# Kernel tuning notes

Measured on AMD Instinct MI355X. Metric: run time of the kernel, lower is better.

Reference implementation:

```python
import jax, jax.numpy as jnp
import numpy as np

NUM_GRAPHS = 256


def _gcn_norm(edge_index, num_nodes):
    # Add self-loops (PyG GCNConv default) and compute symmetric normalization
    loops = jnp.arange(num_nodes, dtype=edge_index.dtype)
    src = jnp.concatenate([edge_index[0], loops])
    dst = jnp.concatenate([edge_index[1], loops])
    deg = jax.ops.segment_sum(jnp.ones_like(dst, dtype=jnp.float32), dst,
                              num_segments=num_nodes)
    dinv = jnp.where(deg > 0, jax.lax.rsqrt(deg), 0.0)
    norm = dinv[src] * dinv[dst]  # [E + N]
    return src, dst, norm


def _gcn_layer(x, W, b, src, dst, norm, num_nodes):
    h = x @ W                      # transform first (cheaper: N x d_out)
    msg = h[src] * norm[:, None]   # gather + per-edge scale  [E+N, d_out]
    agg = jax.ops.segment_sum(msg, dst, num_segments=num_nodes)
    return agg + b


def setup_inputs() -> dict:
    key = jax.random.key(0)
    ks = jax.random.split(key, 12)
    N, E, F_in = 100000, 1600000, 5
    x = jax.random.normal(ks[0], (N, F_in), dtype=jnp.float32)
    edge_index = jax.random.randint(ks[1], (2, E), 0, N, dtype=jnp.int64)
    batch = jnp.sort(jax.random.randint(ks[2], (N,), 0, NUM_GRAPHS, dtype=jnp.int64))

    def glorot(k, fi, fo):
        s = jnp.sqrt(6.0 / (fi + fo))
        return jax.random.uniform(k, (fi, fo), jnp.float32, -s, s)

    return {
        "x": x, "edge_index": edge_index, "batch": batch,
        "W1": glorot(ks[3], F_in, 64), "b1": jnp.zeros((64,), jnp.float32),
        "W2": glorot(ks[4], 64, 128),  "b2": jnp.zeros((128,), jnp.float32),
        "W3": glorot(ks[5], 128, 64),  "b3": jnp.zeros((64,), jnp.float32),
        "Wfc": glorot(ks[6], 64, 1),   "bfc": jnp.zeros((1,), jnp.float32),
    }


def reference(x, edge_index, batch, W1, b1, W2, b2, W3, b3, Wfc, bfc):
    N = x.shape[0]
    src, dst, norm = _gcn_norm(edge_index, N)
    h = jax.nn.relu(_gcn_layer(x, W1, b1, src, dst, norm, N))
    h = jax.nn.relu(_gcn_layer(h, W2, b2, src, dst, norm, N))
    h = jax.nn.relu(_gcn_layer(h, W3, b3, src, dst, norm, N))
    # global mean pool over graph ids
    sums = jax.ops.segment_sum(h, batch, num_segments=NUM_GRAPHS)
    cnts = jax.ops.segment_sum(jnp.ones((N,), jnp.float32), batch,
                               num_segments=NUM_GRAPHS)
    pooled = sums / jnp.maximum(cnts, 1.0)[:, None]   # [G, 64]
    return jax.nn.sigmoid(pooled @ Wfc + bfc)         # [G, 1]
```

## Files before the change

kernel.cpp:

```cpp
#include <hip/hip_runtime.h>
#include <math.h>

#define NG 256
#define NBK 512
#define BCAP 3584

static __device__ __forceinline__ int bucket_lo(int p, int n) {
    return (int)(((long long)p * n + NBK - 1) / NBK);
}

static __device__ __forceinline__ float blo(unsigned u) {
    return __uint_as_float(u << 16);
}
static __device__ __forceinline__ float bhi(unsigned u) {
    return __uint_as_float(u & 0xFFFF0000u);
}
static __device__ __forceinline__ unsigned packbf(float a, float b) {
    unsigned ua = __float_as_uint(a);
    ua = (ua + 0x7FFFu + ((ua >> 16) & 1u)) >> 16;
    unsigned ub = __float_as_uint(b);
    ub = (ub + 0x7FFFu + ((ub >> 16) & 1u)) & 0xFFFF0000u;
    return ua | ub;
}

__global__ void zero_bcur(int* bcur) {
    int i = blockIdx.x * blockDim.x + threadIdx.x;
    if (i < NBK) bcur[i] = i * BCAP;
}

__global__ void bucketA(const int* __restrict__ src, const int* __restrict__ dst,
                        int* bcur, unsigned* stage, int e, int n) {
    __shared__ int cnt[NBK];
    __shared__ int base[NBK];
    int nb = gridDim.x;
    int c0 = (int)((long long)blockIdx.x * e / nb);
    int c1 = (int)((long long)(blockIdx.x + 1) * e / nb);
    for (int k = threadIdx.x; k < NBK; k += blockDim.x) cnt[k] = 0;
    __syncthreads();
    for (int i = c0 + threadIdx.x; i < c1; i += blockDim.x) {
        int d = dst[i];
        int p = (int)((long long)d * NBK / n);
        atomicAdd(&cnt[p], 1);
    }
    __syncthreads();
    for (int k = threadIdx.x; k < NBK; k += blockDim.x)
        base[k] = atomicAdd(&bcur[k], cnt[k]);
    __syncthreads();
    for (int k = threadIdx.x; k < NBK; k += blockDim.x) cnt[k] = 0;
    __syncthreads();
    for (int i = c0 + threadIdx.x; i < c1; i += blockDim.x) {
        int s = src[i], d = dst[i];
        int p = (int)((long long)d * NBK / n);
        int ldst = d - bucket_lo(p, n);
        int lp = atomicAdd(&cnt[p], 1);
        stage[base[p] + lp] = ((unsigned)s << 8) | (unsigned)ldst;
    }
}

__global__ void fillB2(const unsigned* __restrict__ stage,
                       const int* __restrict__ bcur,
                       int* __restrict__ rowptr, float* __restrict__ dinv,
                       int* __restrict__ csrs,
                       const float* __restrict__ x, float* __restrict__ xs,
                       int n, int e) {
    __shared__ int ldeg[256];
    __shared__ int loff[256];
    __shared__ int bstart;
    int p = blockIdx.x;
    int t = threadIdx.x;
    int lo = bucket_lo(p, n), hi = bucket_lo(p + 1, n);
    int nloc = hi - lo;

    {
        int acc = 0;
        for (int k = t; k < p; k += 256) acc += bcur[k] - k * BCAP;
        ldeg[t] = acc;
        __syncthreads();
        for (int off = 128; off > 0; off >>= 1) {
            if (t < off) ldeg[t] += ldeg[t + off];
            __syncthreads();
        }
        if (t == 0) bstart = ldeg[0];
        __syncthreads();
    }

    if (t < 256) ldeg[t] = 0;
    __syncthreads();
    int s0 = p * BCAP, s1 = bcur[p];
    for (int i = s0 + t; i < s1; i += 256)
        atomicAdd(&ldeg[stage[i] & 255u], 1);
    __syncthreads();

    int v = (t < nloc) ? ldeg[t] : 0;
    loff[t] = v;
    __syncthreads();
    for (int off = 1; off < 256; off <<= 1) {
        int u = (t >= off) ? loff[t - off] : 0;
        __syncthreads();
        loff[t] += u;
        __syncthreads();
    }
    if (t < nloc) {
        int start = bstart + loff[t] - v;
        rowptr[lo + t] = start;
        float dv = rsqrtf((float)v + 1.0f);
        dinv[lo + t] = dv;
        const float* xr = x + (size_t)(lo + t) * 5;
        float* xo = xs + (size_t)(lo + t) * 5;
#pragma unroll
        for (int k = 0; k < 5; ++k) xo[k] = xr[k] * dv;
    }
    if (p == NBK - 1 && t == 0) rowptr[n] = e;
    __syncthreads();
    if (t < nloc) ldeg[t] = bstart + loff[t] - v;
    __syncthreads();

    for (int i = s0 + t; i < s1; i += 256) {
        unsigned pk = stage[i];
        int ldst = (int)(pk & 255u);
        int pos = atomicAdd(&ldeg[ldst], 1);
        csrs[pos] = (int)(pk >> 8);
    }
}

__global__ void gather5(const int* __restrict__ rowptr,
                        const int* __restrict__ csrs,
                        const float* __restrict__ dinv,
                        const float* __restrict__ xs,
                        float* __restrict__ z, int n) {
    int i = blockIdx.x * blockDim.x + threadIdx.x;
    if (i >= n) return;
    const float* xr = xs + (size_t)i * 5;
    float4 x4 = *(const float4*)(xr);
    float a0 = x4.x, a1 = x4.y, a2 = x4.z, a3 = x4.w, a4 = xr[4];
    int j = rowptr[i], end = rowptr[i + 1], e1 = end - 1;
    for (; j < end; j += 4) {
        int s[4]; float m[4];
#pragma unroll
        for (int k = 0; k < 4; ++k) {
            int jj = j + k;
            s[k] = csrs[jj <= e1 ? jj : e1];
            m[k] = (jj < end) ? 1.0f : 0.0f;
        }
        float4 r4[4]; float r1[4];
#pragma unroll
        for (int k = 0; k < 4; ++k) {
            const float* r = xs + (size_t)s[k] * 5;
            r4[k] = *(const float4*)(r);
            r1[k] = r[4];
        }
#pragma unroll
        for (int k = 0; k < 4; ++k) {
            a0 = fmaf(m[k], r4[k].x, a0);
            a1 = fmaf(m[k], r4[k].y, a1);
            a2 = fmaf(m[k], r4[k].z, a2);
            a3 = fmaf(m[k], r4[k].w, a3);
            a4 = fmaf(m[k], r1[k], a4);
        }
    }
    float di = dinv[i];
    float* zr = z + (size_t)i * 5;
    zr[0] = a0 * di; zr[1] = a1 * di; zr[2] = a2 * di;
    zr[3] = a3 * di; zr[4] = a4 * di;
}

template<int DOUT, bool BR, bool SCALE, bool OUTBF>
static __device__ __forceinline__ void emit(float o[8], const float* b, int c,
                                            float dsc, void* out, int i) {
    if (BR) {
        float4 b0 = *(const float4*)(b + c * 8);
        float4 b1 = *(const float4*)(b + c * 8 + 4);
        o[0] = fmaxf(o[0] + b0.x, 0.f); o[1] = fmaxf(o[1] + b0.y, 0.f);
        o[2] = fmaxf(o[2] + b0.z, 0.f); o[3] = fmaxf(o[3] + b0.w, 0.f);
        o[4] = fmaxf(o[4] + b1.x, 0.f); o[5] = fmaxf(o[5] + b1.y, 0.f);
        o[6] = fmaxf(o[6] + b1.z, 0.f); o[7] = fmaxf(o[7] + b1.w, 0.f);
    }
    if (SCALE) {
#pragma unroll
        for (int q = 0; q < 8; ++q) o[q] *= dsc;
    }
    if (OUTBF) {
        uint4 pk;
        pk.x = packbf(o[0], o[1]); pk.y = packbf(o[2], o[3]);
        pk.z = packbf(o[4], o[5]); pk.w = packbf(o[6], o[7]);
        *(uint4*)((unsigned*)out + (size_t)i * (DOUT / 2) + c * 4) = pk;
    } else {
        float* op = (float*)out + (size_t)i * DOUT + c * 8;
        float4 o0 = {o[0], o[1], o[2], o[3]};
        float4 o1 = {o[4], o[5], o[6], o[7]};
        *(float4*)(op) = o0;
        *(float4*)(op + 4) = o1;
    }
}

template<int K, int DOUT, bool BR, bool SCALE, bool OUTBF, int NODES>
__global__ void transformB(const float* __restrict__ xin,
                           const float* __restrict__ W,
                           const float* __restrict__ b,
                           const float* __restrict__ dinv,
                           void* __restrict__ out, int n) {
    const int C = DOUT / 8;
    int tid = blockIdx.x * blockDim.x + threadIdx.x;
    int grp = tid / C;
    int c = tid % C;
    int i0 = grp * NODES;
    if (i0 >= n) return;
    float acc[NODES][8];
#pragma unroll
    for (int nn = 0; nn < NODES; ++nn)
#pragma unroll
        for (int q = 0; q < 8; ++q) acc[nn][q] = 0.0f;

    static_assert(K % 4 == 0, "K multiple of 4");
    int idx[NODES];
#pragma unroll
    for (int nn = 0; nn < NODES; ++nn)
        idx[nn] = (i0 + nn < n) ? i0 + nn : n - 1;

    float4 r[NODES];
#pragma unroll
    for (int nn = 0; nn < NODES; ++nn)
        r[nn] = *(const float4*)(xin + (size_t)idx[nn] * K);

    for (int k0 = 0; k0 < K; k0 += 4) {
        float4 rn[NODES];
        if (k0 + 4 < K) {
#pragma unroll
            for (int nn = 0; nn < NODES; ++nn)
                rn[nn] = *(const float4*)(xin + (size_t)idx[nn] * K + k0 + 4);
        }
#pragma unroll
        for (int kk = 0; kk < 4; ++kk) {
            const float* wp = W + (size_t)(k0 + kk) * DOUT + c * 8;
            float4 w0 = *(const float4*)(wp);
            float4 w1 = *(const float4*)(wp + 4);
#pragma unroll
            for (int nn = 0; nn < NODES; ++nn) {
                float v = (&r[nn].x)[kk];
                acc[nn][0] = fmaf(v, w0.x, acc[nn][0]);
                acc[nn][1] = fmaf(v, w0.y, acc[nn][1]);
                acc[nn][2] = fmaf(v, w0.z, acc[nn][2]);
                acc[nn][3] = fmaf(v, w0.w, acc[nn][3]);
                acc[nn][4] = fmaf(v, w1.x, acc[nn][4]);
                acc[nn][5] = fmaf(v, w1.y, acc[nn][5]);
                acc[nn][6] = fmaf(v, w1.z, acc[nn][6]);
                acc[nn][7] = fmaf(v, w1.w, acc[nn][7]);
            }
        }
#pragma unroll
        for (int nn = 0; nn < NODES; ++nn) r[nn] = rn[nn];
    }
#pragma unroll
    for (int nn = 0; nn < NODES; ++nn) {
        if (i0 + nn >= n) break;
        float dsc = SCALE ? dinv[i0 + nn] : 1.0f;
        emit<DOUT, BR, SCALE, OUTBF>(acc[nn], b, c, dsc, out, i0 + nn);
    }
}

template<int DOUT, bool BR, bool SCALE, bool OUTBF, int NODES>
__global__ void transformB5(const float* __restrict__ xin,
                            const float* __restrict__ W,
                            const float* __restrict__ b,
                            const float* __restrict__ dinv,
                            void* __restrict__ out, int n) {
    const int C = DOUT / 8;
    int tid = blockIdx.x * blockDim.x + threadIdx.x;
    int grp = tid / C;
    int c = tid % C;
    int i0 = grp * NODES;
    if (i0 >= n) return;
    float r[NODES][5];
#pragma unroll
    for (int nn = 0; nn < NODES; ++nn) {
        int idx = i0 + nn < n ? i0 + nn : n - 1;
        const float* row = xin + (size_t)idx * 5;
#pragma unroll
        for (int k = 0; k < 5; ++k) r[nn][k] = row[k];
    }
    float acc[NODES][8];
#pragma unroll
    for (int nn = 0; nn < NODES; ++nn)
#pragma unroll
        for (int q = 0; q < 8; ++q) acc[nn][q] = 0.0f;
#pragma unroll
    for (int k = 0; k < 5; ++k) {
        const float* wp = W + (size_t)k * DOUT + c * 8;
        float4 w0 = *(const float4*)(wp);
        float4 w1 = *(const float4*)(wp + 4);
#pragma unroll
        for (int nn = 0; nn < NODES; ++nn) {
            float v = r[nn][k];
            acc[nn][0] = fmaf(v, w0.x, acc[nn][0]);
            acc[nn][1] = fmaf(v, w0.y, acc[nn][1]);
            acc[nn][2] = fmaf(v, w0.z, acc[nn][2]);
            acc[nn][3] = fmaf(v, w0.w, acc[nn][3]);
            acc[nn][4] = fmaf(v, w1.x, acc[nn][4]);
            acc[nn][5] = fmaf(v, w1.y, acc[nn][5]);
            acc[nn][6] = fmaf(v, w1.z, acc[nn][6]);
            acc[nn][7] = fmaf(v, w1.w, acc[nn][7]);
        }
    }
#pragma unroll
    for (int nn = 0; nn < NODES; ++nn) {
        if (i0 + nn >= n) break;
        float dsc = SCALE ? dinv[i0 + nn] : 1.0f;
        emit<DOUT, BR, SCALE, OUTBF>(acc[nn], b, c, dsc, out, i0 + nn);
    }
}

#define ACCA(AA, V) \
    AA[0] += blo(V.x); AA[1] += bhi(V.x); AA[2] += blo(V.y); AA[3] += bhi(V.y); \
    AA[4] += blo(V.z); AA[5] += bhi(V.z); AA[6] += blo(V.w); AA[7] += bhi(V.w);
#define ACCM(AA, V, M) \
    AA[0] = fmaf(M, blo(V.x), AA[0]); AA[1] = fmaf(M, bhi(V.x), AA[1]); \
    AA[2] = fmaf(M, blo(V.y), AA[2]); AA[3] = fmaf(M, bhi(V.y), AA[3]); \
    AA[4] = fmaf(M, blo(V.z), AA[4]); AA[5] = fmaf(M, bhi(V.z), AA[5]); \
    AA[6] = fmaf(M, blo(V.w), AA[6]); AA[7] = fmaf(M, bhi(V.w), AA[7]);

template<bool BR>
__global__ void gatherBF(const int* __restrict__ rowptr,
                         const int* __restrict__ csrs,
                         const float* __restrict__ dinv,
                         const float* __restrict__ b,
                         const unsigned* __restrict__ g,
                         float* __restrict__ z, int n) {
    int tid = blockIdx.x * blockDim.x + threadIdx.x;
    int i = tid >> 3;
    int c = tid & 7;
    if (i >= n) return;
    uint4 sv = *(const uint4*)(g + (size_t)i * 32 + c * 4);
    float a0[8], a1[8], a2[8], a3[8];
    a0[0] = blo(sv.x); a0[1] = bhi(sv.x); a0[2] = blo(sv.y); a0[3] = bhi(sv.y);
    a0[4] = blo(sv.z); a0[5] = bhi(sv.z); a0[6] = blo(sv.w); a0[7] = bhi(sv.w);
#pragma unroll
    for (int q = 0; q < 8; ++q) { a1[q] = 0.0f; a2[q] = 0.0f; a3[q] = 0.0f; }
    int j = rowptr[i], end = rowptr[i + 1];
    for (; j + 8 <= end; j += 8) {
        uint4 v0 = *(const uint4*)(g + (size_t)csrs[j]     * 32 + c * 4);
        uint4 v1 = *(const uint4*)(g + (size_t)csrs[j + 1] * 32 + c * 4);
        uint4 v2 = *(const uint4*)(g + (size_t)csrs[j + 2] * 32 + c * 4);
        uint4 v3 = *(const uint4*)(g + (size_t)csrs[j + 3] * 32 + c * 4);
        uint4 v4 = *(const uint4*)(g + (size_t)csrs[j + 4] * 32 + c * 4);
        uint4 v5 = *(const uint4*)(g + (size_t)csrs[j + 5] * 32 + c * 4);
        uint4 v6 = *(const uint4*)(g + (size_t)csrs[j + 6] * 32 + c * 4);
        uint4 v7 = *(const uint4*)(g + (size_t)csrs[j + 7] * 32 + c * 4);
        ACCA(a0, v0); ACCA(a1, v1); ACCA(a2, v2); ACCA(a3, v3);
        ACCA(a0, v4); ACCA(a1, v5); ACCA(a2, v6); ACCA(a3, v7);
    }
    if (j < end) {
        int e1 = end - 1;
        int sx[8]; float mm[8];
#pragma unroll
        for (int k = 0; k < 8; ++k) {
            int jj = j + k;
            sx[k] = csrs[jj <= e1 ? jj : e1];
            mm[k] = (jj < end) ? 1.0f : 0.0f;
        }
        uint4 v0 = *(const uint4*)(g + (size_t)sx[0] * 32 + c * 4);
        uint4 v1 = *(const uint4*)(g + (size_t)sx[1] * 32 + c * 4);
        uint4 v2 = *(const uint4*)(g + (size_t)sx[2] * 32 + c * 4);
        uint4 v3 = *(const uint4*)(g + (size_t)sx[3] * 32 + c * 4);
        uint4 v4 = *(const uint4*)(g + (size_t)sx[4] * 32 + c * 4);
        uint4 v5 = *(const uint4*)(g + (size_t)sx[5] * 32 + c * 4);
        uint4 v6 = *(const uint4*)(g + (size_t)sx[6] * 32 + c * 4);
        uint4 v7 = *(const uint4*)(g + (size_t)sx[7] * 32 + c * 4);
        ACCM(a0, v0, mm[0]); ACCM(a1, v1, mm[1]);
        ACCM(a2, v2, mm[2]); ACCM(a3, v3, mm[3]);
        ACCM(a0, v4, mm[4]); ACCM(a1, v5, mm[5]);
        ACCM(a2, v6, mm[6]); ACCM(a3, v7, mm[7]);
    }
    float di = dinv[i];
    float o[8];
#pragma unroll
    for (int q = 0; q < 8; ++q) o[q] = di * ((a0[q] + a1[q]) + (a2[q] + a3[q]));
    if (BR) {
        float4 b0 = *(const float4*)(b + c * 8);
        float4 b1 = *(const float4*)(b + c * 8 + 4);
        o[0] = fmaxf(o[0] + b0.x, 0.f); o[1] = fmaxf(o[1] + b0.y, 0.f);
        o[2] = fmaxf(o[2] + b0.z, 0.f); o[3] = fmaxf(o[3] + b0.w, 0.f);
        o[4] = fmaxf(o[4] + b1.x, 0.f); o[5] = fmaxf(o[5] + b1.y, 0.f);
        o[6] = fmaxf(o[6] + b1.z, 0.f); o[7] = fmaxf(o[7] + b1.w, 0.f);
    }
    float* zp = z + (size_t)i * 64 + c * 8;
    float4 z0 = {o[0], o[1], o[2], o[3]};
    float4 z1 = {o[4], o[5], o[6], o[7]};
    *(float4*)(zp) = z0;
    *(float4*)(zp + 4) = z1;
}

__global__ void pool(const float* __restrict__ h3, const int* __restrict__ batch,
                     const float* __restrict__ Wfc, const float* __restrict__ bfc,
                     float* __restrict__ out, int n) {
    int g = blockIdx.x;
    int lane = threadIdx.x & 63;
    int w = threadIdx.x >> 6;
    int lo = 0, hi = n;
    while (lo < hi) { int m = (lo + hi) >> 1; if (batch[m] < g) lo = m + 1; else hi = m; }
    int start = lo;
    hi = n;
    while (lo < hi) { int m = (lo + hi) >> 1; if (batch[m] < g + 1) lo = m + 1; else hi = m; }
    int end = lo;
    float a0 = 0.f, a1 = 0.f, a2 = 0.f, a3 = 0.f;
    int m = start + w;
    for (; m + 12 < end; m += 16) {
        a0 += h3[(size_t)m * 64 + lane];
        a1 += h3[(size_t)(m + 4) * 64 + lane];
        a2 += h3[(size_t)(m + 8) * 64 + lane];
        a3 += h3[(size_t)(m + 12) * 64 + lane];
    }
    for (; m < end; m += 4) a0 += h3[(size_t)m * 64 + lane];
    __shared__ float sh[4][64];
    sh[w][lane] = (a0 + a1) + (a2 + a3);
    __syncthreads();
    if (w == 0) {
        float v = (sh[0][lane] + sh[1][lane]) + (sh[2][lane] + sh[3][lane]);
        float cnt = (float)(end - start);
        v = (v / fmaxf(cnt, 1.0f)) * Wfc[lane];
#pragma unroll
        for (int off = 32; off > 0; off >>= 1) v += __shfl_down(v, off, 64);
        if (lane == 0) out[g] = 1.0f / (1.0f + expf(-(v + bfc[0])));
    }
}

static inline int cdiv(long long a, int b) { return (int)((a + b - 1) / b); }

extern "C" void kernel_launch(void* const* d_in, const int* in_sizes, int n_in,
                              void* d_out, int out_size, void* d_ws, size_t ws_size,
                              hipStream_t stream) {
    const float* x   = (const float*)d_in[0];
    const int*   ei  = (const int*)d_in[1];
    const int*   bat = (const int*)d_in[2];
    const float* W1  = (const float*)d_in[3];
    const float* b1  = (const float*)d_in[4];
    const float* W2  = (const float*)d_in[5];
    const float* b2  = (const float*)d_in[6];
    const float* W3  = (const float*)d_in[7];
    const float* b3  = (const float*)d_in[8];
    const float* Wfc = (const float*)d_in[9];
    const float* bfc = (const float*)d_in[10];
    float* out = (float*)d_out;

    const int N = in_sizes[0] / 5;
    const int E = in_sizes[1] / 2;
    const int* src = ei;
    const int* ds  = ei + E;

    char* wsb = (char*)d_ws;
    size_t off = 0;
#define A256(X) (((X) + (size_t)255) & ~(size_t)255)
    float* dinv   = (float*)(wsb + off); off = A256(off + (size_t)N * 4);
    int*   rowptr = (int*)(wsb + off);   off = A256(off + (size_t)(N + 4) * 4);
    int*   bcur   = (int*)(wsb + off);   off = A256(off + (size_t)NBK * 4);
    int*   csrs   = (int*)(wsb + off);   off = A256(off + (size_t)E * 4);
    float* A      = (float*)(wsb + off); off = A256(off + (size_t)N * 128 * 4);
    float* B      = (float*)(wsb + off);
#undef A256
    unsigned* stage = (unsigned*)A;
    float*    xs    = A + (size_t)(1 << 21);
    float*    z1    = A;
    unsigned* h1bf  = (unsigned*)B;
    float*    z2    = A;
    float*    h2    = B;
    unsigned* t3bf  = (unsigned*)A;
    float*    h3    = B;

    const int Blk = 256;

    zero_bcur<<<2, 256, 0, stream>>>(bcur);
    bucketA<<<256, 256, 0, stream>>>(src, ds, bcur, stage, E, N);
    fillB2<<<NBK, 256, 0, stream>>>(stage, bcur, rowptr, dinv, csrs, x, xs, N, E);

    gather5<<<cdiv(N, Blk), Blk, 0, stream>>>(rowptr, csrs, dinv, xs, z1, N);
    transformB5<64, true, true, true, 2>
        <<<cdiv((long long)cdiv(N, 2) * 8, Blk), Blk, 0, stream>>>(
        z1, W1, b1, dinv, h1bf, N);

    gatherBF<false><<<cdiv((long long)N * 8, Blk), Blk, 0, stream>>>(
        rowptr, csrs, dinv, nullptr, h1bf, z2, N);
    transformB<64, 128, true, false, false, 4>
        <<<cdiv((long long)cdiv(N, 4) * 16, Blk), Blk, 0, stream>>>(
        z2, W2, b2, nullptr, h2, N);

    transformB<128, 64, false, true, true, 4>
        <<<cdiv((long long)cdiv(N, 4) * 8, Blk), Blk, 0, stream>>>(
        h2, W3, nullptr, dinv, t3bf, N);
    gatherBF<true><<<cdiv((long long)N * 8, Blk), Blk, 0, stream>>>(
        rowptr, csrs, dinv, b3, t3bf, h3, N);

    pool<<<NG, 256, 0, stream>>>(h3, bat, Wfc, bfc, out, N);
}
```

Before: 321.2 us.

## Fuse layer-2 gather, W2 transform and W3 transform into one shared-memory kernel

Replaces the separate gatherBF, transformB (64→128) and transformB (128→64) launches with a single layer23 kernel. Each block aggregates 96 nodes into shared memory, applies W2 with bias and ReLU into a bf16 shared buffer, then applies W3 and writes the dinv-scaled bf16 result. This removes the global round trips for z2 (N×64 fp32) and h2 (N×128 fp32) plus two launches. The costs are heavy shared-memory use that limits occupancy, a gather phase that keeps only 256 threads per block busy, and h2 now being rounded to bf16 before the W3 product.

```diff
diff --git a/kernel.cpp b/kernel.cpp
--- a/kernel.cpp
+++ b/kernel.cpp
@@ -4,6 +4,7 @@
 #define NG 256
 #define NBK 512
 #define BCAP 3584
+#define FBN 96
 
 static __device__ __forceinline__ int bucket_lo(int p, int n) {
     return (int)(((long long)p * n + NBK - 1) / NBK);
@@ -193,71 +194,6 @@
     }
 }
 
-template<int K, int DOUT, bool BR, bool SCALE, bool OUTBF, int NODES>
-__global__ void transformB(const float* __restrict__ xin,
-                           const float* __restrict__ W,
-                           const float* __restrict__ b,
-                           const float* __restrict__ dinv,
-                           void* __restrict__ out, int n) {
-    const int C = DOUT / 8;
-    int tid = blockIdx.x * blockDim.x + threadIdx.x;
-    int grp = tid / C;
-    int c = tid % C;
-    int i0 = grp * NODES;
-    if (i0 >= n) return;
-    float acc[NODES][8];
-#pragma unroll
-    for (int nn = 0; nn < NODES; ++nn)
-#pragma unroll
-        for (int q = 0; q < 8; ++q) acc[nn][q] = 0.0f;
-
-    static_assert(K % 4 == 0, "K multiple of 4");
-    int idx[NODES];
-#pragma unroll
-    for (int nn = 0; nn < NODES; ++nn)
-        idx[nn] = (i0 + nn < n) ? i0 + nn : n - 1;
-
-    float4 r[NODES];
-#pragma unroll
-    for (int nn = 0; nn < NODES; ++nn)
-        r[nn] = *(const float4*)(xin + (size_t)idx[nn] * K);
-
-    for (int k0 = 0; k0 < K; k0 += 4) {
-        float4 rn[NODES];
-        if (k0 + 4 < K) {
-#pragma unroll
-            for (int nn = 0; nn < NODES; ++nn)
-                rn[nn] = *(const float4*)(xin + (size_t)idx[nn] * K + k0 + 4);
-        }
-#pragma unroll
-        for (int kk = 0; kk < 4; ++kk) {
-            const float* wp = W + (size_t)(k0 + kk) * DOUT + c * 8;
-            float4 w0 = *(const float4*)(wp);
-            float4 w1 = *(const float4*)(wp + 4);
-#pragma unroll
-            for (int nn = 0; nn < NODES; ++nn) {
-                float v = (&r[nn].x)[kk];
-                acc[nn][0] = fmaf(v, w0.x, acc[nn][0]);
-                acc[nn][1] = fmaf(v, w0.y, acc[nn][1]);
-                acc[nn][2] = fmaf(v, w0.z, acc[nn][2]);
-                acc[nn][3] = fmaf(v, w0.w, acc[nn][3]);
-                acc[nn][4] = fmaf(v, w1.x, acc[nn][4]);
-                acc[nn][5] = fmaf(v, w1.y, acc[nn][5]);
-                acc[nn][6] = fmaf(v, w1.z, acc[nn][6]);
-                acc[nn][7] = fmaf(v, w1.w, acc[nn][7]);
-            }
-        }
-#pragma unroll
-        for (int nn = 0; nn < NODES; ++nn) r[nn] = rn[nn];
-    }
-#pragma unroll
-    for (int nn = 0; nn < NODES; ++nn) {
-        if (i0 + nn >= n) break;
-        float dsc = SCALE ? dinv[i0 + nn] : 1.0f;
-        emit<DOUT, BR, SCALE, OUTBF>(acc[nn], b, c, dsc, out, i0 + nn);
-    }
-}
-
 template<int DOUT, bool BR, bool SCALE, bool OUTBF, int NODES>
 __global__ void transformB5(const float* __restrict__ xin,
                             const float* __restrict__ W,
@@ -318,17 +254,10 @@
     AA[4] = fmaf(M, blo(V.z), AA[4]); AA[5] = fmaf(M, bhi(V.z), AA[5]); \
     AA[6] = fmaf(M, blo(V.w), AA[6]); AA[7] = fmaf(M, bhi(V.w), AA[7]);
 
-template<bool BR>
-__global__ void gatherBF(const int* __restrict__ rowptr,
-                         const int* __restrict__ csrs,
-                         const float* __restrict__ dinv,
-                         const float* __restrict__ b,
-                         const unsigned* __restrict__ g,
-                         float* __restrict__ z, int n) {
-    int tid = blockIdx.x * blockDim.x + threadIdx.x;
-    int i = tid >> 3;
-    int c = tid & 7;
-    if (i >= n) return;
+static __device__ __forceinline__ void gather_row(const int* __restrict__ rowptr,
+                                                  const int* __restrict__ csrs,
+                                                  const unsigned* __restrict__ g,
+                                                  int i, int c, float o[8]) {
     uint4 sv = *(const uint4*)(g + (size_t)i * 32 + c * 4);
     float a0[8], a1[8], a2[8], a3[8];
     a0[0] = blo(sv.x); a0[1] = bhi(sv.x); a0[2] = blo(sv.y); a0[3] = bhi(sv.y);
@@ -370,10 +299,26 @@
         ACCM(a0, v4, mm[4]); ACCM(a1, v5, mm[5]);
         ACCM(a2, v6, mm[6]); ACCM(a3, v7, mm[7]);
     }
+#pragma unroll
+    for (int q = 0; q < 8; ++q) o[q] = (a0[q] + a1[q]) + (a2[q] + a3[q]);
+}
+
+template<bool BR>
+__global__ void gatherBF(const int* __restrict__ rowptr,
+                         const int* __restrict__ csrs,
+                         const float* __restrict__ dinv,
+                         const float* __restrict__ b,
+                         const unsigned* __restrict__ g,
+                         float* __restrict__ z, int n) {
+    int tid = blockIdx.x * blockDim.x + threadIdx.x;
+    int i = tid >> 3;
+    int c = tid & 7;
+    if (i >= n) return;
+    float o[8];
+    gather_row(rowptr, csrs, g, i, c, o);
     float di = dinv[i];
-    float o[8];
-#pragma unroll
-    for (int q = 0; q < 8; ++q) o[q] = di * ((a0[q] + a1[q]) + (a2[q] + a3[q]));
+#pragma unroll
+    for (int q = 0; q < 8; ++q) o[q] *= di;
     if (BR) {
         float4 b0 = *(const float4*)(b + c * 8);
         float4 b1 = *(const float4*)(b + c * 8 + 4);
@@ -387,6 +332,139 @@
     float4 z1 = {o[4], o[5], o[6], o[7]};
     *(float4*)(zp) = z0;
     *(float4*)(zp + 4) = z1;
+}
+
+__global__ void layer23(const int* __restrict__ rowptr,
+                        const int* __restrict__ csrs,
+                        const float* __restrict__ dinv,
+                        const float* __restrict__ b2v,
+                        const unsigned* __restrict__ g,
+                        const float* __restrict__ W2,
+                        const float* __restrict__ W3,
+                        unsigned* __restrict__ t3, int n) {
+    __shared__ float    z2s[FBN][68];
+    __shared__ unsigned h2s[FBN][68];
+    int t = threadIdx.x;
+    int base = blockIdx.x * FBN;
+
+    {
+        int nd = t >> 3, c = t & 7;
+        for (int pass = 0; pass < 3; ++pass) {
+            int lr = pass * 32 + nd;
+            int i = base + lr;
+            if (i < n) {
+                float o[8];
+                gather_row(rowptr, csrs, g, i, c, o);
+                float di = dinv[i];
+                float4 z0 = {o[0] * di, o[1] * di, o[2] * di, o[3] * di};
+                float4 z1 = {o[4] * di, o[5] * di, o[6] * di, o[7] * di};
+                *(float4*)&z2s[lr][c * 8] = z0;
+                *(float4*)&z2s[lr][c * 8 + 4] = z1;
+            }
+        }
+    }
+    __syncthreads();
+
+    {
+        int c2 = t & 15;
+        int ng = t >> 4;
+        float acc[6][8];
+#pragma unroll
+        for (int nn = 0; nn < 6; ++nn)
+#pragma unroll
+            for (int q = 0; q < 8; ++q) acc[nn][q] = 0.0f;
+        for (int k0 = 0; k0 < 64; k0 += 4) {
+            float4 r[6];
+#pragma unroll
+            for (int nn = 0; nn < 6; ++nn)
+                r[nn] = *(const float4*)&z2s[ng + 16 * nn][k0];
+#pragma unroll
+            for (int kk = 0; kk < 4; ++kk) {
+                const float* wp = W2 + (size_t)(k0 + kk) * 128 + c2 * 8;
+                float4 w0 = *(const float4*)(wp);
+                float4 w1 = *(const float4*)(wp + 4);
+#pragma unroll
+                for (int nn = 0; nn < 6; ++nn) {
+                    float v = (&r[nn].x)[kk];
+                    acc[nn][0] = fmaf(v, w0.x, acc[nn][0]);
+                    acc[nn][1] = fmaf(v, w0.y, acc[nn][1]);
+                    acc[nn][2] = fmaf(v, w0.z, acc[nn][2]);
+                    acc[nn][3] = fmaf(v, w0.w, acc[nn][3]);
+                    acc[nn][4] = fmaf(v, w1.x, acc[nn][4]);
+                    acc[nn][5] = fmaf(v, w1.y, acc[nn][5]);
+                    acc[nn][6] = fmaf(v, w1.z, acc[nn][6]);
+                    acc[nn][7] = fmaf(v, w1.w, acc[nn][7]);
+                }
+            }
+        }
+        float4 b0 = *(const float4*)(b2v + c2 * 8);
+        float4 b1 = *(const float4*)(b2v + c2 * 8 + 4);
+#pragma unroll
+        for (int nn = 0; nn < 6; ++nn) {
+            float o[8];
+            o[0] = fmaxf(acc[nn][0] + b0.x, 0.f);
+            o[1] = fmaxf(acc[nn][1] + b0.y, 0.f);
+            o[2] = fmaxf(acc[nn][2] + b0.z, 0.f);
+            o[3] = fmaxf(acc[nn][3] + b0.w, 0.f);
+            o[4] = fmaxf(acc[nn][4] + b1.x, 0.f);
+            o[5] = fmaxf(acc[nn][5] + b1.y, 0.f);
+            o[6] = fmaxf(acc[nn][6] + b1.z, 0.f);
+            o[7] = fmaxf(acc[nn][7] + b1.w, 0.f);
+            uint4 pk;
+            pk.x = packbf(o[0], o[1]); pk.y = packbf(o[2], o[3]);
+            pk.z = packbf(o[4], o[5]); pk.w = packbf(o[6], o[7]);
+            *(uint4*)&h2s[ng + 16 * nn][c2 * 4] = pk;
+        }
+    }
+    __syncthreads();
+
+    {
+        int c3 = t & 7;
+        int ng = t >> 3;
+        float acc[3][8];
+#pragma unroll
+        for (int nn = 0; nn < 3; ++nn)
+#pragma unroll
+            for (int q = 0; q < 8; ++q) acc[nn][q] = 0.0f;
+        for (int k0 = 0; k0 < 128; k0 += 8) {
+            uint4 r[3];
+#pragma unroll
+            for (int nn = 0; nn < 3; ++nn)
+                r[nn] = *(const uint4*)&h2s[ng + 32 * nn][k0 >> 1];
+#pragma unroll
+            for (int kk = 0; kk < 8; ++kk) {
+                const float* wp = W3 + (size_t)(k0 + kk) * 64 + c3 * 8;
+                float4 w0 = *(const float4*)(wp);
+                float4 w1 = *(const float4*)(wp + 4);
+#pragma unroll
+                for (int nn = 0; nn < 3; ++nn) {
+                    unsigned u = (&r[nn].x)[kk >> 1];
+                    float v = (kk & 1) ? bhi(u) : blo(u);
+                    acc[nn][0] = fmaf(v, w0.x, acc[nn][0]);
+                    acc[nn][1] = fmaf(v, w0.y, acc[nn][1]);
+                    acc[nn][2] = fmaf(v, w0.z, acc[nn][2]);
+                    acc[nn][3] = fmaf(v, w0.w, acc[nn][3]);
+                    acc[nn][4] = fmaf(v, w1.x, acc[nn][4]);
+                    acc[nn][5] = fmaf(v, w1.y, acc[nn][5]);
+                    acc[nn][6] = fmaf(v, w1.z, acc[nn][6]);
+                    acc[nn][7] = fmaf(v, w1.w, acc[nn][7]);
+                }
+            }
+        }
+#pragma unroll
+        for (int nn = 0; nn < 3; ++nn) {
+            int i = base + ng + 32 * nn;
+            if (i < n) {
+                float ds = dinv[i];
+                uint4 pk;
+                pk.x = packbf(acc[nn][0] * ds, acc[nn][1] * ds);
+                pk.y = packbf(acc[nn][2] * ds, acc[nn][3] * ds);
+                pk.z = packbf(acc[nn][4] * ds, acc[nn][5] * ds);
+                pk.w = packbf(acc[nn][6] * ds, acc[nn][7] * ds);
+                *(uint4*)(t3 + (size_t)i * 32 + c3 * 4) = pk;
+            }
+        }
+    }
 }
 
 __global__ void pool(const float* __restrict__ h3, const int* __restrict__ batch,
@@ -460,8 +538,6 @@
     float*    xs    = A + (size_t)(1 << 21);
     float*    z1    = A;
     unsigned* h1bf  = (unsigned*)B;
-    float*    z2    = A;
-    float*    h2    = B;
     unsigned* t3bf  = (unsigned*)A;
     float*    h3    = B;
 
@@ -476,15 +552,9 @@
         <<<cdiv((long long)cdiv(N, 2) * 8, Blk), Blk, 0, stream>>>(
         z1, W1, b1, dinv, h1bf, N);
 
-    gatherBF<false><<<cdiv((long long)N * 8, Blk), Blk, 0, stream>>>(
-        rowptr, csrs, dinv, nullptr, h1bf, z2, N);
-    transformB<64, 128, true, false, false, 4>
-        <<<cdiv((long long)cdiv(N, 4) * 16, Blk), Blk, 0, stream>>>(
-        z2, W2, b2, nullptr, h2, N);
-
-    transformB<128, 64, false, true, true, 4>
-        <<<cdiv((long long)cdiv(N, 4) * 8, Blk), Blk, 0, stream>>>(
-        h2, W3, nullptr, dinv, t3bf, N);
+    layer23<<<cdiv(N, FBN), 256, 0, stream>>>(
+        rowptr, csrs, dinv, b2, h1bf, W2, W3, t3bf, N);
+
     gatherBF<true><<<cdiv((long long)N * 8, Blk), Blk, 0, stream>>>(
         rowptr, csrs, dinv, b3, t3bf, h3, N);
 
```

Result: faster. 280.0 us (-12.8%).
